# Kernel optimization log

Hardware: AMD Instinct MI355X
Metric: run time of the kernel (lower is better)

## Reference

```python
import jax, jax.numpy as jnp
import numpy as np

# irreps layout: 64x0e + 64x1o + 64x2e  ->  flattened dim = 64*(1+3+5) = 576
MULS = (64, 64, 64)
DIMS = (1, 3, 5)   # 2l+1 for l = 0, 1, 2
N = 262144


def setup_inputs() -> dict:
    key = jax.random.key(0)
    k0, k1, k2, k3 = jax.random.split(key, 4)
    total = sum(m * d for m, d in zip(MULS, DIMS))  # 576
    x = jax.random.normal(k0, (N, total), dtype=jnp.float32)
    # FunctionalLinear weights: one [mul_in, mul_out] matrix per (irrep_in, irrep_out) path.
    # With gradient_normalization='path', init std = sqrt(alpha)^(1-1) = 1.
    w0 = jax.random.normal(k1, (64, 64), dtype=jnp.float32)
    w1 = jax.random.normal(k2, (64, 64), dtype=jnp.float32)
    w2 = jax.random.normal(k3, (64, 64), dtype=jnp.float32)
    return {"x": x, "w0": w0, "w1": w1, "w2": w2}


def reference(x, w0, w1, w2):
    # e3nn Linear with irreps_in == irreps_out == 64x0e+64x1o+64x2e:
    # per irrep l: out[:, w, i] = sqrt(1/mul_in) * sum_u x[:, u, i] * W[u, w]
    # (path_normalization='element' -> alpha = 1/mul_in; gradient_normalization='path'
    #  -> full sqrt(alpha) applied in the forward pass.)
    ws = (w0, w1, w2)
    outs = []
    off = 0
    for mul, d, w in zip(MULS, DIMS, ws):
        xl = x[..., off:off + mul * d].reshape(x.shape[:-1] + (mul, d))  # [N, mul, 2l+1]
        off += mul * d
        scale = jnp.sqrt(jnp.asarray(1.0 / mul, dtype=x.dtype))
        yl = scale * jnp.einsum('nui,uw->nwi', xl, w)  # small per-irrep matmul
        outs.append(yl.reshape(x.shape[:-1] + (mul * d,)))
    return jnp.concatenate(outs, axis=-1)  # [N, 576]
```

## Files before the change

kernel.cpp:

```cpp
#include <hip/hip_runtime.h>


typedef _Float16 half4  __attribute__((ext_vector_type(4)));
typedef float    f32x4  __attribute__((ext_vector_type(4)));

#define RPB      16
#define NROWS    262144
#define ROWF     576
#define XROWS    (RPB * 9)
#define OUTBYTES (RPB * ROWF * 4)
#define LDS_BYTES OUTBYTES

template<int D, int OFF, int SEGROW, int F4PR>
__device__ __forceinline__ void stage_seg(unsigned char* lds, const float* __restrict__ xrow0, int tid) {
#pragma unroll
  for (int it = 0; it < RPB * F4PR / 256; ++it) {
    int t = tid + it * 256;
    int row = t / F4PR;
    int f4  = t - row * F4PR;
    f32x4 v = *(const f32x4*)(xrow0 + (long long)row * ROWF + OFF + f4 * 4);
    int idx = f4 * 4;
    if (D == 1) {
      int lrow = SEGROW + row;
      int b = (lrow * 128 + idx * 2) ^ ((lrow & 7) << 4);
      half4 h = { (_Float16)v[0], (_Float16)v[1], (_Float16)v[2], (_Float16)v[3] };
      *(half4*)(lds + b) = h;
    } else {
#pragma unroll
      for (int j = 0; j < 4; ++j) {
        int u = (idx + j) / D;
        int i = (idx + j) - u * D;
        int lrow = SEGROW + row * D + i;
        int b = (lrow * 128 + u * 2) ^ ((lrow & 7) << 4);
        *(_Float16*)(lds + b) = (_Float16)v[j];
      }
    }
  }
}

__device__ __forceinline__ void load_bfrag(const float* __restrict__ W, int wt,
                                           int lane15, int laneq, half4 bf[4]) {
  int w = wt * 16 + lane15;
#pragma unroll
  for (int s = 0; s < 4; ++s) {
    int u0 = s * 16 + laneq * 4;
#pragma unroll
    for (int j = 0; j < 4; ++j)
      bf[s][j] = (_Float16)W[(u0 + j) * 64 + w];
  }
}

template<int SEGROW, int MT>
__device__ __forceinline__ void compute_seg(const unsigned char* lds, int lane15, int laneq,
                                            const half4 bf[4], f32x4 acc[MT]) {
  const int coff = laneq * 8;
#pragma unroll
  for (int mt = 0; mt < MT; ++mt) {
    int arow  = SEGROW + mt * 16 + lane15;
    int abase = arow * 128;
    int aswz  = (arow & 7) << 4;
    acc[mt] = (f32x4){0.f, 0.f, 0.f, 0.f};
#pragma unroll
    for (int s = 0; s < 4; ++s) {
      half4 a = *(const half4*)(lds + abase + ((s * 32 + coff) ^ aswz));
      acc[mt] = __builtin_amdgcn_mfma_f32_16x16x16f16(a, bf[s], acc[mt], 0, 0, 0);
    }
  }
}

template<int D, int OFF, int MT>
__device__ __forceinline__ void scatter_seg(unsigned char* lds, int wt, int lane15, int laneq,
                                            const f32x4 acc[MT]) {
  const int w = wt * 16 + lane15;
#pragma unroll
  for (int mt = 0; mt < MT; ++mt) {
#pragma unroll
    for (int j = 0; j < 4; ++j) {
      int r = mt * 16 + laneq * 4 + j;
      int n = r / D;
      int i = r - n * D;
      *(float*)(lds + n * (ROWF * 4) + (OFF + w * D + i) * 4) = 0.125f * acc[mt][j];
    }
  }
}

__global__ __launch_bounds__(256, 4) void linear_irreps(
    const float* __restrict__ x,
    const float* __restrict__ w0, const float* __restrict__ w1, const float* __restrict__ w2,
    float* __restrict__ out) {
  __shared__ __align__(16) unsigned char lds[LDS_BYTES];
  const int tid = threadIdx.x;
  const int lane = tid & 63, wave = tid >> 6;
  const int lane15 = lane & 15, laneq = lane >> 4;
  const int wt = wave;
  const long long base = (long long)blockIdx.x * (RPB * ROWF);

  half4 bf0[4], bf1[4], bf2[4];
  load_bfrag(w0, wt, lane15, laneq, bf0);
  load_bfrag(w1, wt, lane15, laneq, bf1);
  load_bfrag(w2, wt, lane15, laneq, bf2);

  stage_seg<1,   0,   0, 16>(lds, x + base, tid);
  stage_seg<3,  64,  16, 48>(lds, x + base, tid);
  stage_seg<5, 256,  64, 80>(lds, x + base, tid);
  __syncthreads();

  f32x4 acc1[1], acc3[3], acc5[5];
  compute_seg<  0, 1>(lds, lane15, laneq, bf0, acc1);
  compute_seg< 16, 3>(lds, lane15, laneq, bf1, acc3);
  compute_seg< 64, 5>(lds, lane15, laneq, bf2, acc5);
  __syncthreads();

  scatter_seg<1,   0, 1>(lds, wt, lane15, laneq, acc1);
  scatter_seg<3,  64, 3>(lds, wt, lane15, laneq, acc3);
  scatter_seg<5, 256, 5>(lds, wt, lane15, laneq, acc5);
  __syncthreads();

#pragma unroll
  for (int k = 0; k < OUTBYTES / 4096; ++k) {
    int q = tid + k * 256;
    f32x4 v = *(const f32x4*)(lds + q * 16);
    *(f32x4*)(out + base + q * 4) = v;
  }
}

extern "C" void kernel_launch(void* const* d_in, const int* in_sizes, int n_in,
                              void* d_out, int out_size, void* d_ws, size_t ws_size,
                              hipStream_t stream) {
  const float* x  = (const float*)d_in[0];
  const float* w0 = (const float*)d_in[1];
  const float* w1 = (const float*)d_in[2];
  const float* w2 = (const float*)d_in[3];
  float* out = (float*)d_out;
  linear_irreps<<<NROWS / RPB, 256, 0, stream>>>(x, w0, w1, w2, out);
}
```

Measured before the change: 248.4 us.

## Use per-wave output strips in LDS to drop final barrier, add nontemporal stores

Each wave now writes its MFMA results into its own private LDS strip, holding its 16 output columns for every irrep across all 16 rows, using an XOR swizzle. Because the wave then reads back only its own strip, the block-wide barrier before the global store is removed. The final writes become nontemporal 16-byte stores. The trade-off is that each wave writes shorter, scattered 16-byte pieces per row instead of the whole block writing fully contiguous rows, which may coalesce less well.

```diff
diff --git a/kernel.cpp b/kernel.cpp
--- a/kernel.cpp
+++ b/kernel.cpp
@@ -7,9 +7,8 @@
 #define RPB      16
 #define NROWS    262144
 #define ROWF     576
-#define XROWS    (RPB * 9)
-#define OUTBYTES (RPB * ROWF * 4)
-#define LDS_BYTES OUTBYTES
+#define STRIP_B  9216
+#define LDS_BYTES (4 * STRIP_B)
 
 template<int D, int OFF, int SEGROW, int F4PR>
 __device__ __forceinline__ void stage_seg(unsigned char* lds, const float* __restrict__ xrow0, int tid) {
@@ -68,10 +67,9 @@
   }
 }
 
-template<int D, int OFF, int MT>
-__device__ __forceinline__ void scatter_seg(unsigned char* lds, int wt, int lane15, int laneq,
-                                            const f32x4 acc[MT]) {
-  const int w = wt * 16 + lane15;
+template<int D, int SOFF, int MT>
+__device__ __forceinline__ void scatter_strip(unsigned char* strip, int lane15, int laneq,
+                                              const f32x4 acc[MT]) {
 #pragma unroll
   for (int mt = 0; mt < MT; ++mt) {
 #pragma unroll
@@ -79,7 +77,9 @@
       int r = mt * 16 + laneq * 4 + j;
       int n = r / D;
       int i = r - n * D;
-      *(float*)(lds + n * (ROWF * 4) + (OFF + w * D + i) * 4) = 0.125f * acc[mt][j];
+      int col = SOFF + lane15 * D + i;
+      int b = (n * 576 + col * 4) ^ ((n & 7) << 4);
+      *(float*)(strip + b) = 0.125f * acc[mt][j];
     }
   }
 }
@@ -111,16 +111,21 @@
   compute_seg< 64, 5>(lds, lane15, laneq, bf2, acc5);
   __syncthreads();
 
-  scatter_seg<1,   0, 1>(lds, wt, lane15, laneq, acc1);
-  scatter_seg<3,  64, 3>(lds, wt, lane15, laneq, acc3);
-  scatter_seg<5, 256, 5>(lds, wt, lane15, laneq, acc5);
-  __syncthreads();
+  unsigned char* strip = lds + wt * STRIP_B;
+  scatter_strip<1,   0, 1>(strip, lane15, laneq, acc1);
+  scatter_strip<3,  16, 3>(strip, lane15, laneq, acc3);
+  scatter_strip<5,  64, 5>(strip, lane15, laneq, acc5);
 
 #pragma unroll
-  for (int k = 0; k < OUTBYTES / 4096; ++k) {
-    int q = tid + k * 256;
-    f32x4 v = *(const f32x4*)(lds + q * 16);
-    *(f32x4*)(out + base + q * 4) = v;
+  for (int k = 0; k < 9; ++k) {
+    int t = lane + k * 64;
+    int n = t / 36;
+    int q = t - n * 36;
+    int goff = (q < 4)  ? wt * 16 + q * 4
+             : (q < 16) ? 64  + wt * 48 + (q - 4) * 4
+                        : 256 + wt * 80 + (q - 16) * 4;
+    f32x4 v = *(const f32x4*)(strip + ((n * 576 + q * 16) ^ ((n & 7) << 4)));
+    __builtin_nontemporal_store(v, (f32x4*)(out + base + n * ROWF + goff));
   }
 }
 
```

Result: slower. 258.0 us (+3.9%).
